# Kernel optimization log

Hardware: AMD Instinct MI355X
Metric: run time of the kernel (lower is better)

The kernel has to match this reference:

```python
import jax, jax.numpy as jnp
import numpy as np

L, DIRS, H, I, B, T = 2, 2, 512, 1024, 64, 1024


def _gru_dir(x_seq, h0, w_ih, w_hh, b_ih, b_hh, reverse):
    """Run one GRU direction. x_seq: (B,T,in), h0: (B,H). Returns (out (B,T,H), h_T (B,H))."""
    # Precompute input projections for all timesteps: (T,B,3H)
    gi = jnp.einsum('bti,gi->tbg', x_seq, w_ih) + b_ih

    def step(h, gi_t):
        gh = h @ w_hh.T + b_hh                      # (B,3H)
        i_r, i_z, i_n = jnp.split(gi_t, 3, axis=-1)
        h_r, h_z, h_n = jnp.split(gh, 3, axis=-1)
        r = jax.nn.sigmoid(i_r + h_r)
        z = jax.nn.sigmoid(i_z + h_z)
        n = jnp.tanh(i_n + r * h_n)
        h_new = (1.0 - z) * n + z * h
        return h_new, h_new

    h_T, out = jax.lax.scan(step, h0, gi, reverse=reverse)
    return out.transpose(1, 0, 2), h_T            # (B,T,H), (B,H)


def setup_inputs() -> dict:
    key = jax.random.key(0)
    ks = jax.random.split(key, 6)
    s = 1.0 / np.sqrt(H)  # PyTorch-style init scale, avoids gate saturation
    return {
        'x':    jax.random.normal(ks[0], (B, T, I), jnp.float32),
        'h0':   jax.random.normal(ks[1], (L * DIRS, B, H), jnp.float32) * s,
        'w_ih': jax.random.normal(ks[2], (L, DIRS, 3 * H, I), jnp.float32) * s,
        'w_hh': jax.random.normal(ks[3], (L, DIRS, 3 * H, H), jnp.float32) * s,
        'b_ih': jax.random.normal(ks[4], (L, DIRS, 3 * H), jnp.float32) * s,
        'b_hh': jax.random.normal(ks[5], (L, DIRS, 3 * H), jnp.float32) * s,
    }


def reference(x, h0, w_ih, w_hh, b_ih, b_hh):
    layer_in = x
    h_finals = []
    for l in range(L):  # small fixed loop over structurally distinct layers
        out_f, hT_f = _gru_dir(layer_in, h0[2 * l],     w_ih[l, 0], w_hh[l, 0], b_ih[l, 0], b_hh[l, 0], reverse=False)
        out_b, hT_b = _gru_dir(layer_in, h0[2 * l + 1], w_ih[l, 1], w_hh[l, 1], b_ih[l, 1], b_hh[l, 1], reverse=True)
        layer_in = jnp.concatenate([out_f, out_b], axis=-1)  # (B,T,2H)
        h_finals.extend([hT_f, hT_b])
    h_n = jnp.stack(h_finals, axis=0)  # (L*2, B, H), PyTorch ordering
    return layer_in, h_n
```

## Files before the change

### kernel.cpp

```cpp
#include <hip/hip_runtime.h>
#include <stdint.h>
#include <stdio.h>

#define TL 1024
#define BB 64
#define HH 512
#define II 1024
#define NL 2
#define BT_ (BB*TL)
#define G3_ 1536
#define N2_ 3072

typedef _Float16 h8 __attribute__((ext_vector_type(8)));
typedef _Float16 h4 __attribute__((ext_vector_type(4)));
typedef _Float16 h2 __attribute__((ext_vector_type(2)));
typedef float    f4 __attribute__((ext_vector_type(4)));
typedef unsigned int u4 __attribute__((ext_vector_type(4)));
typedef unsigned int u2v __attribute__((ext_vector_type(2)));

__global__ void cvt_f2h(const float* __restrict__ src, _Float16* __restrict__ dst, size_t n4) {
  size_t i = (size_t)blockIdx.x*blockDim.x + threadIdx.x;
  size_t stride = (size_t)gridDim.x*blockDim.x;
  for (; i < n4; i += stride) {
    f4 v = ((const f4*)src)[i];
    h4 o;
    o[0] = (_Float16)v[0]; o[1] = (_Float16)v[1];
    o[2] = (_Float16)v[2]; o[3] = (_Float16)v[3];
    ((h4*)dst)[i] = o;
  }
}

#define LDA 40
__launch_bounds__(256)
__global__ void gemm_gi(const _Float16* __restrict__ A, const _Float16* __restrict__ Bw,
                        const float* __restrict__ bias, _Float16* __restrict__ gi)
{
  const int bn = blockIdx.x, bm = blockIdx.y;
  const int tid = threadIdx.x;
  const int wave = tid >> 6, lane = tid & 63;
  const int wm = wave >> 1, wn = wave & 1;
  const int lo = lane & 15, hi = lane >> 4;
  __shared__ _Float16 As[128*LDA];
  __shared__ _Float16 Bs[128*LDA];
  f4 acc[4][4] = {};
  const int r0 = tid >> 2, c0 = (tid & 3)*8;
  const _Float16* Ag = A + (size_t)(bm*128)*II;
  const _Float16* Bg = Bw + (size_t)(bn*128)*II;
  u4 a0 = *(const u4*)(Ag + (size_t)r0*II + c0);
  u4 a1 = *(const u4*)(Ag + (size_t)(64+r0)*II + c0);
  u4 b0 = *(const u4*)(Bg + (size_t)r0*II + c0);
  u4 b1 = *(const u4*)(Bg + (size_t)(64+r0)*II + c0);
  for (int kt = 0; kt < 32; ++kt) {
    __syncthreads();
    *(u4*)&As[r0*LDA + c0] = a0;
    *(u4*)&As[(64+r0)*LDA + c0] = a1;
    *(u4*)&Bs[r0*LDA + c0] = b0;
    *(u4*)&Bs[(64+r0)*LDA + c0] = b1;
    if (kt+1 < 32) {
      const int off = (kt+1)*32 + c0;
      a0 = *(const u4*)(Ag + (size_t)r0*II + off);
      a1 = *(const u4*)(Ag + (size_t)(64+r0)*II + off);
      b0 = *(const u4*)(Bg + (size_t)r0*II + off);
      b1 = *(const u4*)(Bg + (size_t)(64+r0)*II + off);
    }
    __syncthreads();
    h8 af[4], bf[4];
    #pragma unroll
    for (int i = 0; i < 4; ++i)
      af[i] = *(const h8*)&As[(wm*64 + i*16 + lo)*LDA + hi*8];
    #pragma unroll
    for (int j = 0; j < 4; ++j)
      bf[j] = *(const h8*)&Bs[(wn*64 + j*16 + lo)*LDA + hi*8];
    #pragma unroll
    for (int i = 0; i < 4; ++i)
      #pragma unroll
      for (int j = 0; j < 4; ++j)
        acc[i][j] = __builtin_amdgcn_mfma_f32_16x16x32_f16(af[i], bf[j], acc[i][j], 0, 0, 0);
  }
  const int nbase = bn*128 + wn*64;
  const int mbase = bm*128 + wm*64;
  #pragma unroll
  for (int j = 0; j < 4; ++j) {
    int n = nbase + j*16 + lo;
    int dir = (n >= G3_) ? 1 : 0;
    int row = n - dir*G3_;
    float bs = bias[n];
    #pragma unroll
    for (int i = 0; i < 4; ++i) {
      int m0 = mbase + i*16 + hi*4;
      #pragma unroll
      for (int v = 0; v < 4; ++v)
        gi[((size_t)dir*BT_ + (size_t)(m0+v))*G3_ + row] = (_Float16)(acc[i][j][v] + bs);
    }
  }
}

#define LDW 520
__launch_bounds__(512, 1)
__global__ void gru_layer(const _Float16* __restrict__ gi,
                          const _Float16* __restrict__ whh,
                          const float* __restrict__ bhh,
                          const float* __restrict__ h0,
                          unsigned long long* __restrict__ tagh,
                          _Float16* __restrict__ out_mid,
                          float* __restrict__ out_fin,
                          float* __restrict__ hn_out,
                          int layer)
{
  const int bid = blockIdx.x;
  const int gg = bid & 7, d = gg & 1, g = gg >> 1;
  const int member = bid >> 3;
  const int j0 = member * 32, b0 = g * 16;
  const int tid = threadIdx.x;
  const int wave = tid >> 6, lane = tid & 63, lo = lane & 15, hi = lane >> 4;
  const int gate = wave >> 1, jh = wave & 1;

  __shared__ _Float16 wlds[3][32][LDW];
  __shared__ _Float16 hlds[16][LDW];
  __shared__ float    ghlds[3][32][17];
  __shared__ _Float16 gil[2][16][3][32];

  const _Float16* wsrc = whh + (size_t)d*G3_*HH;
  #pragma unroll
  for (int it = 0; it < 12; ++it) {
    int idx = it*512 + tid;
    int row = idx >> 6;
    int c8 = (idx & 63) * 8;
    int gt = row >> 5, jj = row & 31;
    u4 v = *(const u4*)(wsrc + (size_t)(gt*HH + j0 + jj)*HH + c8);
    *(u4*)&wlds[gt][jj][c8] = v;
  }

  const int ejp = tid & 15;
  const int eb  = tid >> 4;
  const bool ew = (tid < 256);
  const int ejA = j0 + 2*ejp;

  unsigned long long* Tb = tagh + (size_t)d*2*BB*256;

  float hj[2];
  float bhr[2], bhz[2], bhn[2];
  unsigned long long E[16];

  if (ew) {
    #pragma unroll
    for (int u = 0; u < 2; ++u) {
      bhr[u] = bhh[(size_t)d*G3_ + 0*HH + ejA + u];
      bhz[u] = bhh[(size_t)d*G3_ + 1*HH + ejA + u];
      bhn[u] = bhh[(size_t)d*G3_ + 2*HH + ejA + u];
      hj[u]  = h0[((size_t)(2*layer + d)*BB + b0 + eb)*HH + ejA + u];
    }
    h2 p; p[0] = (_Float16)hj[0]; p[1] = (_Float16)hj[1];
    unsigned long long ent = (unsigned long long)__builtin_bit_cast(unsigned, p) | (1ull << 32);
    unsigned long long* ptr = Tb + (size_t)0*BB*256 + (size_t)(b0 + eb)*256 + (member*16 + ejp);
    __hip_atomic_store(ptr, ent, __ATOMIC_RELAXED, __HIP_MEMORY_SCOPE_AGENT);
    const unsigned long long* Trd = Tb;
    #pragma unroll
    for (int q = 0; q < 4; ++q)
      #pragma unroll
      for (int k = 0; k < 4; ++k) {
        int i = tid*2 + (k >> 1);
        E[q*4+k] = __hip_atomic_load(
            Trd + (size_t)(b0 + (i >> 5))*256 + q*64 + (i & 31)*2 + (k & 1),
            __ATOMIC_RELAXED, __HIP_MEMORY_SCOPE_AGENT);
      }
  }
  if (wave >= 6) {
    const int t0 = d ? (TL-1) : 0;
    const int L = tid - 384;
    #pragma unroll
    for (int r = 0; r < 2; ++r) {
      int idx = L + r*128;
      if (idx < 192) {
        int seg = idx >> 2, q = idx & 3;
        int gt = seg >> 4, b = seg & 15;
        u4 v = *(const u4*)(gi + (size_t)d*BT_*G3_ + ((size_t)(b0+b)*TL + t0)*G3_ + gt*HH + j0 + q*8);
        *(u4*)&gil[0][b][gt][q*8] = v;
      }
    }
  }
  __syncthreads();

  for (int s = 0; s < TL; ++s) {
    const int t = d ? (TL-1 - s) : s;
    const int rpar = s & 1, wpar = rpar ^ 1;
    const unsigned tgt = (unsigned)(s + 1);
    const unsigned long long* Trd = Tb + (size_t)rpar*BB*256;

    if (wave < 6) {
      if (ew) {
        for (;;) {
          unsigned ok = 1u;
          #pragma unroll
          for (int k = 0; k < 16; ++k)
            ok &= (unsigned)((E[k] >> 32) >= tgt);
          if (ok) break;
          #pragma unroll
          for (int q = 0; q < 4; ++q)
            #pragma unroll
            for (int k = 0; k < 4; ++k) {
              int i = tid*2 + (k >> 1);
              E[q*4+k] = __hip_atomic_load(
                  Trd + (size_t)(b0 + (i >> 5))*256 + q*64 + (i & 31)*2 + (k & 1),
                  __ATOMIC_RELAXED, __HIP_MEMORY_SCOPE_AGENT);
            }
        }
        #pragma unroll
        for (int q = 0; q < 4; ++q)
          #pragma unroll
          for (int k = 0; k < 2; ++k) {
            int i = tid*2 + k;
            int b = i >> 5, p = i & 31;
            u2v dv; dv[0] = (unsigned)E[q*4 + k*2]; dv[1] = (unsigned)E[q*4 + k*2 + 1];
            *(u2v*)&hlds[b][q*128 + p*4] = dv;
          }
      }
      asm volatile("s_waitcnt lgkmcnt(0)" ::: "memory");
      __builtin_amdgcn_s_barrier();
      __builtin_amdgcn_sched_barrier(0);
      f4 acc = {0.f, 0.f, 0.f, 0.f};
      #pragma unroll
      for (int kk = 0; kk < 16; ++kk) {
        h8 af = *(const h8*)&hlds[lo][kk*32 + hi*8];
        h8 bf = *(const h8*)&wlds[gate][jh*16 + lo][kk*32 + hi*8];
        acc = __builtin_amdgcn_mfma_f32_16x16x32_f16(af, bf, acc, 0, 0, 0);
      }
      #pragma unroll
      for (int v = 0; v < 4; ++v)
        ghlds[gate][jh*16 + lo][hi*4 + v] = acc[v];
      asm volatile("s_waitcnt lgkmcnt(0)" ::: "memory");
      __builtin_amdgcn_s_barrier();
      __builtin_amdgcn_sched_barrier(0);
      if (ew) {
        unsigned giR = *(const unsigned*)&gil[rpar][eb][0][2*ejp];
        unsigned giZ = *(const unsigned*)&gil[rpar][eb][1][2*ejp];
        unsigned giN = *(const unsigned*)&gil[rpar][eb][2][2*ejp];
        h2 pR = __builtin_bit_cast(h2, giR);
        h2 pZ = __builtin_bit_cast(h2, giZ);
        h2 pN = __builtin_bit_cast(h2, giN);
        h2 hnew; float hv[2];
        #pragma unroll
        for (int u = 0; u < 2; ++u) {
          float ir = (float)pR[u], iz = (float)pZ[u], inn = (float)pN[u];
          float hr = ghlds[0][2*ejp+u][eb] + bhr[u];
          float hz = ghlds[1][2*ejp+u][eb] + bhz[u];
          float hn = ghlds[2][2*ejp+u][eb] + bhn[u];
          float rr = 1.f/(1.f + __expf(-(ir + hr)));
          float zz = 1.f/(1.f + __expf(-(iz + hz)));
          float xx = inn + rr*hn;
          float nn = 1.f - 2.f/(__expf(2.f*xx) + 1.f);
          float h  = (1.f - zz)*nn + zz*hj[u];
          hj[u] = h; hnew[u] = (_Float16)h; hv[u] = h;
        }
        unsigned hu = __builtin_bit_cast(unsigned, hnew);
        unsigned long long ent = (unsigned long long)hu | ((unsigned long long)(s + 2) << 32);
        unsigned long long* ptr = Tb + (size_t)wpar*BB*256 + (size_t)(b0 + eb)*256 + (member*16 + ejp);
        __hip_atomic_store(ptr, ent, __ATOMIC_RELAXED, __HIP_MEMORY_SCOPE_AGENT);
        if (out_mid) {
          *(unsigned*)(out_mid + ((size_t)(b0+eb)*TL + t)*(size_t)(2*HH) + d*HH + ejA) = hu;
        } else {
          u2v ov; ov[0] = __builtin_bit_cast(unsigned, hv[0]); ov[1] = __builtin_bit_cast(unsigned, hv[1]);
          *(u2v*)(out_fin + ((size_t)(b0+eb)*TL + t)*(size_t)(2*HH) + d*HH + ejA) = ov;
        }
        const unsigned long long* Trn = Tb + (size_t)wpar*BB*256;
        #pragma unroll
        for (int q = 0; q < 4; ++q)
          #pragma unroll
          for (int k = 0; k < 4; ++k) {
            int i = tid*2 + (k >> 1);
            E[q*4+k] = __hip_atomic_load(
                Trn + (size_t)(b0 + (i >> 5))*256 + q*64 + (i & 31)*2 + (k & 1),
                __ATOMIC_RELAXED, __HIP_MEMORY_SCOPE_AGENT);
          }
      }
    } else {
      const int L = tid - 384;
      u4 va = {}, vb = {};
      int have = 0;
      if (s + 1 < TL) {
        const int tn = d ? (TL-1 - (s+1)) : (s+1);
        const _Float16* gbase = gi + (size_t)d*BT_*G3_ + (size_t)0;
        {
          int idx = L;
          int seg = idx >> 2, q = idx & 3;
          int gt = seg >> 4, b = seg & 15;
          va = *(const u4*)(gbase + ((size_t)(b0+b)*TL + tn)*G3_ + gt*HH + j0 + q*8);
        }
        if (L < 64) {
          int idx = L + 128;
          int seg = idx >> 2, q = idx & 3;
          int gt = seg >> 4, b = seg & 15;
          vb = *(const u4*)(gbase + ((size_t)(b0+b)*TL + tn)*G3_ + gt*HH + j0 + q*8);
        }
        have = 1;
      }
      __builtin_amdgcn_s_barrier();
      if (have) {
        const int wbuf = wpar;
        {
          int idx = L;
          int seg = idx >> 2, q = idx & 3;
          int gt = seg >> 4, b = seg & 15;
          *(u4*)&gil[wbuf][b][gt][q*8] = va;
        }
        if (L < 64) {
          int idx = L + 128;
          int seg = idx >> 2, q = idx & 3;
          int gt = seg >> 4, b = seg & 15;
          *(u4*)&gil[wbuf][b][gt][q*8] = vb;
        }
      }
      asm volatile("s_waitcnt lgkmcnt(0)" ::: "memory");
      __builtin_amdgcn_s_barrier();
    }
  }
  if (ew) {
    #pragma unroll
    for (int u = 0; u < 2; ++u)
      hn_out[((size_t)(2*layer + d)*BB + b0 + eb)*HH + ejA + u] = hj[u];
  }
}

extern "C" void kernel_launch(void* const* d_in, const int* in_sizes, int n_in,
                              void* d_out, int out_size, void* d_ws, size_t ws_size,
                              hipStream_t stream) {
  (void)in_sizes; (void)n_in; (void)out_size;
  const float* x   = (const float*)d_in[0];
  const float* h0  = (const float*)d_in[1];
  const float* wih = (const float*)d_in[2];
  const float* whh = (const float*)d_in[3];
  const float* bih = (const float*)d_in[4];
  const float* bhh = (const float*)d_in[5];
  float* out = (float*)d_out;

  char* ws = (char*)d_ws;
  size_t off = 0;
  auto alloc = [&](size_t bytes) {
    char* p = ws + off;
    off += (bytes + 255) & ~(size_t)255;
    return p;
  };
  _Float16* x16   = (_Float16*)alloc((size_t)BT_*II*2);
  _Float16* mid16 = (_Float16*)alloc((size_t)BT_*II*2);
  _Float16* gi16  = (_Float16*)alloc((size_t)2*BT_*G3_*2);
  _Float16* wih16 = (_Float16*)alloc((size_t)NL*N2_*II*2);
  _Float16* whh16 = (_Float16*)alloc((size_t)NL*N2_*HH*2);
  unsigned long long* tagh = (unsigned long long*)alloc((size_t)NL*2*2*BB*256*8);
  if (off > ws_size) {
    fprintf(stderr, "kernel_launch: workspace too small: need %zu have %zu\n", off, ws_size);
    return;
  }

  hipMemsetAsync(tagh, 0, (size_t)NL*2*2*BB*256*8, stream);
  cvt_f2h<<<2048, 256, 0, stream>>>(x,   x16,   (size_t)BT_*II/4);
  cvt_f2h<<<512,  256, 0, stream>>>(wih, wih16, (size_t)NL*N2_*II/4);
  cvt_f2h<<<512,  256, 0, stream>>>(whh, whh16, (size_t)NL*N2_*HH/4);

  float* hn = out + (size_t)BT_*II;

  gemm_gi<<<dim3(24, 512), 256, 0, stream>>>(x16, wih16, bih, gi16);
  gru_layer<<<128, 512, 0, stream>>>(gi16, whh16, bhh, h0, tagh,
                                     mid16, nullptr, hn, 0);
  gemm_gi<<<dim3(24, 512), 256, 0, stream>>>(mid16, wih16 + (size_t)N2_*II, bih + N2_, gi16);
  gru_layer<<<128, 512, 0, stream>>>(gi16, whh16 + (size_t)N2_*HH, bhh + N2_, h0,
                                     tagh + (size_t)2*2*BB*256, nullptr, out, hn, 1);
}
```

Before: 8.177 ms.

## Offload output stores to loader waves and deepen gi prefetch to two steps

Compute waves now stage each new hidden state in LDS instead of writing it to global output on the serial recurrence path. The loader waves write the previous step's outputs to global memory after the barrier, and a final flush handles the last timestep. The gi prefetch is also restructured to a two-step register pipeline, so loads for step s+2 are issued right after step s+1 is committed to LDS. This takes global store latency off the critical dependency chain, at the cost of extra LDS traffic and more work for the loader waves.

```diff
diff --git a/kernel.cpp b/kernel.cpp
--- a/kernel.cpp
+++ b/kernel.cpp
@@ -119,6 +119,7 @@
   __shared__ _Float16 hlds[16][LDW];
   __shared__ float    ghlds[3][32][17];
   __shared__ _Float16 gil[2][16][3][32];
+  __shared__ u2v      olds[256];
 
   const _Float16* wsrc = whh + (size_t)d*G3_*HH;
   #pragma unroll
@@ -141,42 +142,47 @@
   float hj[2];
   float bhr[2], bhz[2], bhn[2];
   unsigned long long E[16];
-
-  if (ew) {
-    #pragma unroll
-    for (int u = 0; u < 2; ++u) {
-      bhr[u] = bhh[(size_t)d*G3_ + 0*HH + ejA + u];
-      bhz[u] = bhh[(size_t)d*G3_ + 1*HH + ejA + u];
-      bhn[u] = bhh[(size_t)d*G3_ + 2*HH + ejA + u];
-      hj[u]  = h0[((size_t)(2*layer + d)*BB + b0 + eb)*HH + ejA + u];
-    }
-    h2 p; p[0] = (_Float16)hj[0]; p[1] = (_Float16)hj[1];
-    unsigned long long ent = (unsigned long long)__builtin_bit_cast(unsigned, p) | (1ull << 32);
-    unsigned long long* ptr = Tb + (size_t)0*BB*256 + (size_t)(b0 + eb)*256 + (member*16 + ejp);
-    __hip_atomic_store(ptr, ent, __ATOMIC_RELAXED, __HIP_MEMORY_SCOPE_AGENT);
-    const unsigned long long* Trd = Tb;
-    #pragma unroll
-    for (int q = 0; q < 4; ++q)
-      #pragma unroll
-      for (int k = 0; k < 4; ++k) {
-        int i = tid*2 + (k >> 1);
-        E[q*4+k] = __hip_atomic_load(
-            Trd + (size_t)(b0 + (i >> 5))*256 + q*64 + (i & 31)*2 + (k & 1),
-            __ATOMIC_RELAXED, __HIP_MEMORY_SCOPE_AGENT);
-      }
-  }
-  if (wave >= 6) {
+  u4 vc0 = {}, vc1 = {};
+  const int L = tid - 384;
+
+  if (wave < 6) {
+    if (ew) {
+      #pragma unroll
+      for (int u = 0; u < 2; ++u) {
+        bhr[u] = bhh[(size_t)d*G3_ + 0*HH + ejA + u];
+        bhz[u] = bhh[(size_t)d*G3_ + 1*HH + ejA + u];
+        bhn[u] = bhh[(size_t)d*G3_ + 2*HH + ejA + u];
+        hj[u]  = h0[((size_t)(2*layer + d)*BB + b0 + eb)*HH + ejA + u];
+      }
+      h2 p; p[0] = (_Float16)hj[0]; p[1] = (_Float16)hj[1];
+      unsigned long long ent = (unsigned long long)__builtin_bit_cast(unsigned, p) | (1ull << 32);
+      unsigned long long* ptr = Tb + (size_t)0*BB*256 + (size_t)(b0 + eb)*256 + (member*16 + ejp);
+      __hip_atomic_store(ptr, ent, __ATOMIC_RELAXED, __HIP_MEMORY_SCOPE_AGENT);
+      #pragma unroll
+      for (int q = 0; q < 4; ++q)
+        #pragma unroll
+        for (int k = 0; k < 4; ++k) {
+          int i = tid*2 + (k >> 1);
+          E[q*4+k] = __hip_atomic_load(
+              Tb + (size_t)(b0 + (i >> 5))*256 + q*64 + (i & 31)*2 + (k & 1),
+              __ATOMIC_RELAXED, __HIP_MEMORY_SCOPE_AGENT);
+        }
+    }
+  } else {
     const int t0 = d ? (TL-1) : 0;
-    const int L = tid - 384;
-    #pragma unroll
-    for (int r = 0; r < 2; ++r) {
-      int idx = L + r*128;
-      if (idx < 192) {
-        int seg = idx >> 2, q = idx & 3;
-        int gt = seg >> 4, b = seg & 15;
-        u4 v = *(const u4*)(gi + (size_t)d*BT_*G3_ + ((size_t)(b0+b)*TL + t0)*G3_ + gt*HH + j0 + q*8);
-        *(u4*)&gil[0][b][gt][q*8] = v;
-      }
+    const int t1 = d ? (TL-2) : 1;
+    {
+      int seg = L >> 2, q = L & 3, gt = seg >> 4, b = seg & 15;
+      u4 v = *(const u4*)(gi + (size_t)d*BT_*G3_ + ((size_t)(b0+b)*TL + t0)*(size_t)G3_ + gt*HH + j0 + q*8);
+      *(u4*)&gil[0][b][gt][q*8] = v;
+      vc0 = *(const u4*)(gi + (size_t)d*BT_*G3_ + ((size_t)(b0+b)*TL + t1)*(size_t)G3_ + gt*HH + j0 + q*8);
+    }
+    if (L < 64) {
+      int i1 = L + 128;
+      int seg = i1 >> 2, q = i1 & 3, gt = seg >> 4, b = seg & 15;
+      u4 v = *(const u4*)(gi + (size_t)d*BT_*G3_ + ((size_t)(b0+b)*TL + t0)*(size_t)G3_ + gt*HH + j0 + q*8);
+      *(u4*)&gil[0][b][gt][q*8] = v;
+      vc1 = *(const u4*)(gi + (size_t)d*BT_*G3_ + ((size_t)(b0+b)*TL + t1)*(size_t)G3_ + gt*HH + j0 + q*8);
     }
   }
   __syncthreads();
@@ -185,10 +191,10 @@
     const int t = d ? (TL-1 - s) : s;
     const int rpar = s & 1, wpar = rpar ^ 1;
     const unsigned tgt = (unsigned)(s + 1);
-    const unsigned long long* Trd = Tb + (size_t)rpar*BB*256;
 
     if (wave < 6) {
       if (ew) {
+        const unsigned long long* Trd = Tb + (size_t)rpar*BB*256;
         for (;;) {
           unsigned ok = 1u;
           #pragma unroll
@@ -253,15 +259,13 @@
           hj[u] = h; hnew[u] = (_Float16)h; hv[u] = h;
         }
         unsigned hu = __builtin_bit_cast(unsigned, hnew);
+        u2v ov;
+        if (out_mid) { ov[0] = hu; ov[1] = hu; }
+        else { ov[0] = __builtin_bit_cast(unsigned, hv[0]); ov[1] = __builtin_bit_cast(unsigned, hv[1]); }
+        olds[tid] = ov;
         unsigned long long ent = (unsigned long long)hu | ((unsigned long long)(s + 2) << 32);
         unsigned long long* ptr = Tb + (size_t)wpar*BB*256 + (size_t)(b0 + eb)*256 + (member*16 + ejp);
         __hip_atomic_store(ptr, ent, __ATOMIC_RELAXED, __HIP_MEMORY_SCOPE_AGENT);
-        if (out_mid) {
-          *(unsigned*)(out_mid + ((size_t)(b0+eb)*TL + t)*(size_t)(2*HH) + d*HH + ejA) = hu;
-        } else {
-          u2v ov; ov[0] = __builtin_bit_cast(unsigned, hv[0]); ov[1] = __builtin_bit_cast(unsigned, hv[1]);
-          *(u2v*)(out_fin + ((size_t)(b0+eb)*TL + t)*(size_t)(2*HH) + d*HH + ejA) = ov;
-        }
         const unsigned long long* Trn = Tb + (size_t)wpar*BB*256;
         #pragma unroll
         for (int q = 0; q < 4; ++q)
@@ -274,44 +278,66 @@
           }
       }
     } else {
-      const int L = tid - 384;
-      u4 va = {}, vb = {};
-      int have = 0;
-      if (s + 1 < TL) {
-        const int tn = d ? (TL-1 - (s+1)) : (s+1);
-        const _Float16* gbase = gi + (size_t)d*BT_*G3_ + (size_t)0;
+      __builtin_amdgcn_s_barrier();
+      __builtin_amdgcn_sched_barrier(0);
+      {
+        int seg = L >> 2, q = L & 3, gt = seg >> 4, b = seg & 15;
+        *(u4*)&gil[wpar][b][gt][q*8] = vc0;
+      }
+      if (L < 64) {
+        int i1 = L + 128;
+        int seg = i1 >> 2, q = i1 & 3, gt = seg >> 4, b = seg & 15;
+        *(u4*)&gil[wpar][b][gt][q*8] = vc1;
+      }
+      {
+        int sn = (s + 2 < TL) ? s + 2 : TL - 1;
+        int tn = d ? (TL-1 - sn) : sn;
+        int seg = L >> 2, q = L & 3, gt = seg >> 4, b = seg & 15;
+        vc0 = *(const u4*)(gi + (size_t)d*BT_*G3_ + ((size_t)(b0+b)*TL + tn)*(size_t)G3_ + gt*HH + j0 + q*8);
+        if (L < 64) {
+          int i1 = L + 128;
+          int seg1 = i1 >> 2, q1 = i1 & 3, gt1 = seg1 >> 4, b1 = seg1 & 15;
+          vc1 = *(const u4*)(gi + (size_t)d*BT_*G3_ + ((size_t)(b0+b1)*TL + tn)*(size_t)G3_ + gt1*HH + j0 + q1*8);
+        }
+      }
+      if (s > 0) {
+        int tp = d ? (TL-1 - (s-1)) : (s-1);
         {
-          int idx = L;
-          int seg = idx >> 2, q = idx & 3;
-          int gt = seg >> 4, b = seg & 15;
-          va = *(const u4*)(gbase + ((size_t)(b0+b)*TL + tn)*G3_ + gt*HH + j0 + q*8);
-        }
-        if (L < 64) {
-          int idx = L + 128;
-          int seg = idx >> 2, q = idx & 3;
-          int gt = seg >> 4, b = seg & 15;
-          vb = *(const u4*)(gbase + ((size_t)(b0+b)*TL + tn)*G3_ + gt*HH + j0 + q*8);
-        }
-        have = 1;
-      }
-      __builtin_amdgcn_s_barrier();
-      if (have) {
-        const int wbuf = wpar;
+          int b = L >> 4, jp = L & 15;
+          u2v o0 = olds[L];
+          if (out_mid) *(unsigned*)(out_mid + ((size_t)(b0+b)*TL + tp)*(size_t)(2*HH) + d*HH + j0 + 2*jp) = o0[0];
+          else         *(u2v*)(out_fin + ((size_t)(b0+b)*TL + tp)*(size_t)(2*HH) + d*HH + j0 + 2*jp) = o0;
+        }
         {
-          int idx = L;
-          int seg = idx >> 2, q = idx & 3;
-          int gt = seg >> 4, b = seg & 15;
-          *(u4*)&gil[wbuf][b][gt][q*8] = va;
-        }
-        if (L < 64) {
-          int idx = L + 128;
-          int seg = idx >> 2, q = idx & 3;
-          int gt = seg >> 4, b = seg & 15;
-          *(u4*)&gil[wbuf][b][gt][q*8] = vb;
+          int i1 = L + 128;
+          int b = i1 >> 4, jp = i1 & 15;
+          u2v o1 = olds[i1];
+          if (out_mid) *(unsigned*)(out_mid + ((size_t)(b0+b)*TL + tp)*(size_t)(2*HH) + d*HH + j0 + 2*jp) = o1[0];
+          else         *(u2v*)(out_fin + ((size_t)(b0+b)*TL + tp)*(size_t)(2*HH) + d*HH + j0 + 2*jp) = o1;
         }
       }
       asm volatile("s_waitcnt lgkmcnt(0)" ::: "memory");
       __builtin_amdgcn_s_barrier();
+      __builtin_amdgcn_sched_barrier(0);
+    }
+  }
+  asm volatile("s_waitcnt lgkmcnt(0)" ::: "memory");
+  __builtin_amdgcn_s_barrier();
+  __builtin_amdgcn_sched_barrier(0);
+  if (wave >= 6) {
+    int tp = d ? 0 : (TL-1);
+    {
+      int b = L >> 4, jp = L & 15;
+      u2v o0 = olds[L];
+      if (out_mid) *(unsigned*)(out_mid + ((size_t)(b0+b)*TL + tp)*(size_t)(2*HH) + d*HH + j0 + 2*jp) = o0[0];
+      else         *(u2v*)(out_fin + ((size_t)(b0+b)*TL + tp)*(size_t)(2*HH) + d*HH + j0 + 2*jp) = o0;
+    }
+    {
+      int i1 = L + 128;
+      int b = i1 >> 4, jp = i1 & 15;
+      u2v o1 = olds[i1];
+      if (out_mid) *(unsigned*)(out_mid + ((size_t)(b0+b)*TL + tp)*(size_t)(2*HH) + d*HH + j0 + 2*jp) = o1[0];
+      else         *(u2v*)(out_fin + ((size_t)(b0+b)*TL + tp)*(size_t)(2*HH) + d*HH + j0 + 2*jp) = o1;
     }
   }
   if (ew) {
```

Result: slower. 9.100 ms (+11.3%).
